# Kernel tuning notes

Measured on AMD Instinct MI355X. Metric: run time of the kernel, lower is better.

The kernel has to match this reference:

```python
import jax, jax.numpy as jnp
import numpy as np

D_MODEL, HEAD_DIM = 1024, 128

def setup_inputs() -> dict:
    key = jax.random.key(0)
    kx, kq, kk, kv = jax.random.split(key, 4)
    x = jax.random.normal(kx, (4, 4096, D_MODEL), dtype=jnp.float32)
    s = 1.0 / np.sqrt(D_MODEL)
    Wq = jax.random.normal(kq, (D_MODEL, HEAD_DIM), dtype=jnp.float32) * s
    Wk = jax.random.normal(kk, (D_MODEL, HEAD_DIM), dtype=jnp.float32) * s
    Wv = jax.random.normal(kv, (D_MODEL, HEAD_DIM), dtype=jnp.float32) * s
    return {"x": x, "Wq": Wq, "Wk": Wk, "Wv": Wv}

def reference(x, Wq, Wk, Wv):
    # x: [b, s, d_model]; Wq/Wk/Wv: [d_model, head_dim]
    q = jnp.einsum('bsd,dh->bsh', x, Wq)
    k = jnp.einsum('bsd,dh->bsh', x, Wk)
    v = jnp.einsum('bsd,dh->bsh', x, Wv)
    seq = x.shape[1]
    scale = 1.0 / jnp.sqrt(jnp.asarray(q.shape[-1], q.dtype))
    scores = jnp.einsum('bqh,bkh->bqk', q, k) * scale  # [b, s, s]
    causal = jnp.tril(jnp.ones((seq, seq), dtype=bool))
    scores = jnp.where(causal, scores, jnp.asarray(-jnp.inf, scores.dtype))
    attn = jax.nn.softmax(scores, axis=-1)
    return jnp.einsum('bqk,bkh->bqh', attn, v)
```

## Files before the change

kernel.cpp:

```cpp
#include <hip/hip_runtime.h>
#include <hip/hip_bf16.h>
#include <math.h>

#define D_MODEL 1024
#define HD 128
#define SEQ 4096

typedef __bf16 bf16x8 __attribute__((ext_vector_type(8)));
typedef float f32x4 __attribute__((ext_vector_type(4)));
typedef unsigned int u32;
typedef u32 u32x4 __attribute__((ext_vector_type(4)));

__device__ __forceinline__ unsigned short f2bf(float f) {
    union { float f; u32 u; } c; c.f = f;
    u32 u = c.u;
    u = (u + 0x7fffu + ((u >> 16) & 1u)) >> 16;
    return (unsigned short)u;
}
__device__ __forceinline__ u32 pk2(float a, float b) {
    __hip_bfloat162 h = __float22bfloat162_rn(make_float2(a, b));
    union { __hip_bfloat162 h; u32 u; } c; c.h = h; return c.u;
}
__device__ __forceinline__ void dma16(void* lds, const void* g) {
    __builtin_amdgcn_global_load_lds(
        (const __attribute__((address_space(1))) u32*)g,
        (__attribute__((address_space(3))) u32*)lds, 16, 0, 0);
}
__device__ __forceinline__ void drain_dma()  { __builtin_amdgcn_s_waitcnt(0x0F70); }
__device__ __forceinline__ void drain_dma4() { __builtin_amdgcn_s_waitcnt(0x0F74); }

__global__ __launch_bounds__(256)
void wt_kernel(const float* __restrict__ Wq, const float* __restrict__ Wk,
               const float* __restrict__ Wv, unsigned short* __restrict__ Wt) {
    __shared__ float wsf[64][129];
    const int t = threadIdx.x;
    const int k0 = blockIdx.x * 64;
    const int mat = blockIdx.y;
    const float* W = (mat == 0) ? Wq : (mat == 1) ? Wk : Wv;
    const float sc = (mat == 0) ? (0.08838834764831845f * 1.4426950408889634f) : 1.0f;
    {
        const int r = t >> 2, c = (t & 3) * 32;
        const float* src = W + (size_t)(k0 + r) * HD + c;
        #pragma unroll
        for (int j = 0; j < 32; j += 4)
            *reinterpret_cast<f32x4*>(&wsf[r][c + j]) = *reinterpret_cast<const f32x4*>(src + j);
    }
    __syncthreads();
    const int n = t >> 1, ks = (t & 1) * 32;
    u32 ow[16];
    #pragma unroll
    for (int j = 0; j < 16; ++j)
        ow[j] = pk2(wsf[ks + 2 * j][n] * sc, wsf[ks + 2 * j + 1][n] * sc);
    unsigned short* dst = Wt + (size_t)(mat * HD + n) * D_MODEL + k0 + ks;
    #pragma unroll
    for (int j = 0; j < 4; ++j)
        *reinterpret_cast<u32x4*>(dst + j * 8) = (u32x4){ow[4*j], ow[4*j+1], ow[4*j+2], ow[4*j+3]};
}

__global__ __launch_bounds__(256)
void proj_kernel(const float* __restrict__ x, const unsigned short* __restrict__ Wt,
                 unsigned short* __restrict__ Qb, unsigned short* __restrict__ Kb,
                 unsigned short* __restrict__ Vt) {
    __shared__ __align__(1024) char ps[49152];
    const int t = threadIdx.x;
    const int w = t >> 6, l = t & 63, li = l & 15, g2 = l >> 4;
    const int id = blockIdx.x;
    const int grp = id / 24, win = id % 24;
    const int nbase = (win >> 3) * 128;
    const int rowbase = (grp * 8 + (win & 7)) * 64;

    f32x4 acc[8];
    #pragma unroll
    for (int nt = 0; nt < 8; ++nt) acc[nt] = (f32x4){0.f, 0.f, 0.f, 0.f};

    const int lrow = l >> 3;
    const int xg = (l & 7) ^ (lrow & 6);
    const int wgr = (l & 7) ^ lrow;
    const int wrow_add = (wgr >> 2) << 6;
    const int wkc = (wgr & 3) * 8;

    auto stage = [&](int k0, int buf) {
        #pragma unroll
        for (int j = 0; j < 2; ++j) {
            int r0 = w * 16 + 8 * j;
            dma16(ps + buf * 8192 + r0 * 128,
                  x + (size_t)(rowbase + r0 + lrow) * D_MODEL + k0 + xg * 4);
            dma16(ps + 24576 + buf * 8192 + r0 * 128,
                  Wt + (size_t)(nbase + r0 + lrow + wrow_add) * D_MODEL + k0 + wkc);
        }
    };

    stage(0, 0);
    stage(32, 1);
    for (int it = 0; it < 32; ++it) {
        const int buf = it % 3;
        if (it < 31) drain_dma4(); else drain_dma();
        __syncthreads();
        if (it + 2 < 32) stage((it + 2) * 32, (it + 2) % 3);
        const char* xb = ps + buf * 8192 + (w * 16 + li) * 128 + (((2 * g2) ^ (li & 6)) * 16);
        f32x4 x0 = *reinterpret_cast<const f32x4*>(xb);
        f32x4 x1 = *reinterpret_cast<const f32x4*>(xb + 16);
        union { u32 d[4]; bf16x8 v; } cva;
        cva.d[0] = pk2(x0[0], x0[1]); cva.d[1] = pk2(x0[2], x0[3]);
        cva.d[2] = pk2(x1[0], x1[1]); cva.d[3] = pk2(x1[2], x1[3]);
        bf16x8 af = cva.v;
        #pragma unroll
        for (int nt = 0; nt < 8; ++nt) {
            bf16x8 bfr = *reinterpret_cast<const bf16x8*>(
                ps + 24576 + buf * 8192 + ((nt & 3) * 16 + li) * 128 +
                ((((nt >> 2) * 4 + g2) ^ (li & 7)) * 16));
            acc[nt] = __builtin_amdgcn_mfma_f32_16x16x32_bf16(af, bfr, acc[nt], 0, 0, 0);
        }
    }

    if (nbase < 256) {
        unsigned short* P = nbase ? Kb : Qb;
        #pragma unroll
        for (int nt = 0; nt < 8; ++nt)
            #pragma unroll
            for (int r = 0; r < 4; ++r) {
                int grow = rowbase + w * 16 + g2 * 4 + r;
                P[(size_t)grow * HD + nt * 16 + li] = f2bf(acc[nt][r]);
            }
    } else {
        int grow0 = rowbase + w * 16 + g2 * 4;
        int b_ = grow0 >> 12, s_ = grow0 & 4095;
        #pragma unroll
        for (int nt = 0; nt < 8; ++nt) {
            ushort4 s4;
            s4.x = f2bf(acc[nt][0]); s4.y = f2bf(acc[nt][1]);
            s4.z = f2bf(acc[nt][2]); s4.w = f2bf(acc[nt][3]);
            *reinterpret_cast<ushort4*>(&Vt[((size_t)b_ * HD + nt * 16 + li) * SEQ + s_]) = s4;
        }
    }
}

__global__ __launch_bounds__(256, 2)
void attn_kernel(const unsigned short* __restrict__ Qb, const unsigned short* __restrict__ Kb,
                 const unsigned short* __restrict__ Vt, float* __restrict__ outO,
                 unsigned short* __restrict__ Obf, float* __restrict__ Lbuf) {
    __shared__ __align__(1024) char smem[36864];
    const int t = threadIdx.x;
    const int w = t >> 6, l = t & 63, li = l & 15, g2 = l >> 4;
    const int b = blockIdx.x & 3;
    const int u = blockIdx.x >> 2;
    const int g = 63 - (u >> 2);
    const int c = u & 3;
    const int R = 2 * g + 2;
    const int ts = (c * R) >> 2, te = ((c + 1) * R) >> 2;
    const int q0 = g * 64;
    const size_t rowb = (size_t)b * SEQ;
    const int qloc = w * 16 + li;

    const unsigned short* KbB = Kb + rowb * HD;
    const unsigned short* VtB = Vt + (size_t)b * HD * SEQ;

    auto stage = [&](int it, char* base) {
        const int j0 = it * 32;
        #pragma unroll
        for (int j = 0; j < 2; ++j) {
            int rK = w * 8 + 4 * j + (l >> 4);
            dma16(base + (w * 8 + 4 * j) * 256,
                  KbB + (size_t)(j0 + rK) * HD + (((l & 15) ^ (rK & 7)) * 8));
            int rV = w * 32 + 16 * j + (l >> 2);
            dma16(base + 8192 + (w * 32 + 16 * j) * 64,
                  VtB + (size_t)rV * SEQ + j0 + (((l & 3) ^ ((l >> 4) & 3)) * 8));
        }
    };

    bf16x8 qf[4];
    #pragma unroll
    for (int ks = 0; ks < 4; ++ks)
        qf[ks] = *reinterpret_cast<const bf16x8*>(
            Qb + (rowb + q0 + qloc) * HD + ks * 32 + g2 * 8);

    f32x4 acco[8];
    #pragma unroll
    for (int dt = 0; dt < 8; ++dt) acco[dt] = (f32x4){0.f, 0.f, 0.f, 0.f};
    float ls = 0.f;

    if (ts < te) stage(ts, smem);
    for (int it = ts; it < te; ++it) {
        char* cbuf = smem + ((it - ts) & 1) * 16384;
        char* nbuf = smem + (((it - ts) & 1) ^ 1) * 16384;
        drain_dma();
        __syncthreads();
        if (it + 1 < te) stage(it + 1, nbuf);

        f32x4 accs[2] = {{0.f,0.f,0.f,0.f}, {0.f,0.f,0.f,0.f}};
        #pragma unroll
        for (int kt = 0; kt < 2; ++kt) {
            const char* kb = cbuf + (kt * 16 + li) * 256;
            #pragma unroll
            for (int ks = 0; ks < 4; ++ks) {
                bf16x8 kf = *reinterpret_cast<const bf16x8*>(kb + (((4 * ks + g2) ^ (li & 7)) * 16));
                accs[kt] = __builtin_amdgcn_mfma_f32_16x16x32_bf16(kf, qf[ks], accs[kt], 0, 0, 0);
            }
        }

        const bool masked = (it >= 2 * g);
        #pragma unroll
        for (int kt = 0; kt < 2; ++kt) {
            float p[4];
            #pragma unroll
            for (int r = 0; r < 4; ++r) {
                float s = accs[kt][r];
                if (masked && ((it - 2 * g) * 32 + kt * 16 + g2 * 4 + r > qloc)) s = -INFINITY;
                p[r] = __builtin_amdgcn_exp2f(s - 16.0f);
                ls += p[r];
            }
            union { u32 d[2]; uint2 v; } pw;
            pw.d[0] = pk2(p[0], p[1]); pw.d[1] = pk2(p[2], p[3]);
            int gq = kt * 2 + (g2 >> 1);
            *reinterpret_cast<uint2*>(
                smem + 32768 + qloc * 64 + ((gq ^ (li & 3)) * 16) + (g2 & 1) * 8) = pw.v;
        }

        bf16x8 pb = *reinterpret_cast<const bf16x8*>(
            smem + 32768 + qloc * 64 + ((g2 ^ (li & 3)) * 16));
        #pragma unroll
        for (int dt = 0; dt < 8; ++dt) {
            bf16x8 va = *reinterpret_cast<const bf16x8*>(
                cbuf + 8192 + (dt * 16 + li) * 64 + ((g2 ^ (li >> 2)) * 16));
            acco[dt] = __builtin_amdgcn_mfma_f32_16x16x32_bf16(va, pb, acco[dt], 0, 0, 0);
        }
    }

    ls += __shfl_xor(ls, 16);
    ls += __shfl_xor(ls, 32);
    if (l < 16)
        Lbuf[(size_t)c * 16384 + rowb + q0 + w * 16 + l] = ls;

    const size_t qrow = rowb + q0 + qloc;
    #pragma unroll
    for (int dt = 0; dt < 8; ++dt) {
        if (c == 3) {
            *reinterpret_cast<f32x4*>(&outO[qrow * HD + dt * 16 + g2 * 4]) = acco[dt];
        } else {
            union { u32 d[2]; uint2 v; } pkd;
            pkd.d[0] = pk2(acco[dt][0], acco[dt][1]);
            pkd.d[1] = pk2(acco[dt][2], acco[dt][3]);
            *reinterpret_cast<uint2*>(
                &Obf[(size_t)c * 2097152 + qrow * HD + dt * 16 + g2 * 4]) = pkd.v;
        }
    }
}

__global__ __launch_bounds__(256)
void merge_kernel(float* __restrict__ outO, const unsigned short* __restrict__ Obf,
                  const float* __restrict__ Lbuf) {
    int tid = blockIdx.x * 256 + threadIdx.x;
    #pragma unroll
    for (int k = 0; k < 4; ++k) {
        int idx = tid + k * 131072;
        int row = idx >> 5, col = (idx & 31) * 4;
        float lsum = Lbuf[row] + Lbuf[16384 + row] + Lbuf[32768 + row] + Lbuf[49152 + row];
        float inv = 1.f / lsum;
        f32x4 o = *reinterpret_cast<const f32x4*>(&outO[(size_t)row * HD + col]);
        #pragma unroll
        for (int cc = 0; cc < 3; ++cc) {
            ushort4 uu = *reinterpret_cast<const ushort4*>(
                &Obf[(size_t)cc * 2097152 + (size_t)row * HD + col]);
            union { u32 u; float f; } a, b2, c2, d2;
            a.u = (u32)uu.x << 16; b2.u = (u32)uu.y << 16;
            c2.u = (u32)uu.z << 16; d2.u = (u32)uu.w << 16;
            o[0] += a.f; o[1] += b2.f; o[2] += c2.f; o[3] += d2.f;
        }
        #pragma unroll
        for (int j = 0; j < 4; ++j) o[j] *= inv;
        *reinterpret_cast<f32x4*>(&outO[(size_t)row * HD + col]) = o;
    }
}

extern "C" void kernel_launch(void* const* d_in, const int* in_sizes, int n_in,
                              void* d_out, int out_size, void* d_ws, size_t ws_size,
                              hipStream_t stream) {
    const float* x  = (const float*)d_in[0];
    const float* Wq = (const float*)d_in[1];
    const float* Wk = (const float*)d_in[2];
    const float* Wv = (const float*)d_in[3];
    float* out = (float*)d_out;

    char* ws = (char*)d_ws;
    unsigned short* Qb  = (unsigned short*)(ws);
    unsigned short* Kb  = (unsigned short*)(ws + ((size_t)4  << 20));
    unsigned short* Vt  = (unsigned short*)(ws + ((size_t)8  << 20));
    unsigned short* Wt  = (unsigned short*)(ws + ((size_t)12 << 20));
    unsigned short* Obf = (unsigned short*)(ws + ((size_t)13 << 20));
    float*          Lb  = (float*)(ws + ((size_t)25 << 20));

    wt_kernel   <<<dim3(16, 3), dim3(256), 0, stream>>>(Wq, Wk, Wv, Wt);
    proj_kernel <<<dim3(768),   dim3(256), 0, stream>>>(x, Wt, Qb, Kb, Vt);
    attn_kernel <<<dim3(1024),  dim3(256), 0, stream>>>(Qb, Kb, Vt, out, Obf, Lb);
    merge_kernel<<<dim3(512),   dim3(256), 0, stream>>>(out, Obf, Lb);
}
```

Before: 171.8 us.

## Fuse split-KV merge into attention kernel via last-block atomic counter

Removes the separate merge kernel launch. Each attention block bumps a per-query-tile atomic counter after a release fence, and the fourth block to finish combines the four partial outputs and row sums for its 64 query rows. The counters are zeroed in the weight-transpose kernel. This saves a launch and lets the merge overlap with the tail of the attention work, at the cost of atomics, fences and an extra tail on some blocks.

Result: slower. 316.6 us (+84.3%).

```diff
diff --git a/kernel.cpp b/kernel.cpp
--- a/kernel.cpp
+++ b/kernel.cpp
@@ -31,9 +31,11 @@
 
 __global__ __launch_bounds__(256)
 void wt_kernel(const float* __restrict__ Wq, const float* __restrict__ Wk,
-               const float* __restrict__ Wv, unsigned short* __restrict__ Wt) {
+               const float* __restrict__ Wv, unsigned short* __restrict__ Wt,
+               int* __restrict__ cnt) {
     __shared__ float wsf[64][129];
     const int t = threadIdx.x;
+    if (blockIdx.x == 0 && blockIdx.y == 0) cnt[t] = 0;
     const int k0 = blockIdx.x * 64;
     const int mat = blockIdx.y;
     const float* W = (mat == 0) ? Wq : (mat == 1) ? Wk : Wv;
@@ -138,7 +140,8 @@
 __global__ __launch_bounds__(256, 2)
 void attn_kernel(const unsigned short* __restrict__ Qb, const unsigned short* __restrict__ Kb,
                  const unsigned short* __restrict__ Vt, float* __restrict__ outO,
-                 unsigned short* __restrict__ Obf, float* __restrict__ Lbuf) {
+                 unsigned short* __restrict__ Obf, float* __restrict__ Lbuf,
+                 int* __restrict__ cnt) {
     __shared__ __align__(1024) char smem[36864];
     const int t = threadIdx.x;
     const int w = t >> 6, l = t & 63, li = l & 15, g2 = l >> 4;
@@ -244,23 +247,30 @@
                 &Obf[(size_t)c * 2097152 + qrow * HD + dt * 16 + g2 * 4]) = pkd.v;
         }
     }
-}
-
-__global__ __launch_bounds__(256)
-void merge_kernel(float* __restrict__ outO, const unsigned short* __restrict__ Obf,
-                  const float* __restrict__ Lbuf) {
-    int tid = blockIdx.x * 256 + threadIdx.x;
-    #pragma unroll
-    for (int k = 0; k < 4; ++k) {
-        int idx = tid + k * 131072;
+
+    __builtin_amdgcn_fence(__ATOMIC_RELEASE, "agent");
+    __syncthreads();
+    __shared__ int lastf;
+    const int gidx = ((u >> 2) << 2) | b;
+    if (t == 0)
+        lastf = (__hip_atomic_fetch_add(&cnt[gidx], 1, __ATOMIC_ACQ_REL,
+                                        __HIP_MEMORY_SCOPE_AGENT) == 3);
+    __syncthreads();
+    if (!lastf) return;
+    __builtin_amdgcn_fence(__ATOMIC_ACQUIRE, "agent");
+
+    #pragma unroll
+    for (int k = 0; k < 8; ++k) {
+        int idx = t + k * 256;
         int row = idx >> 5, col = (idx & 31) * 4;
-        float lsum = Lbuf[row] + Lbuf[16384 + row] + Lbuf[32768 + row] + Lbuf[49152 + row];
+        size_t grow = rowb + q0 + row;
+        float lsum = Lbuf[grow] + Lbuf[16384 + grow] + Lbuf[32768 + grow] + Lbuf[49152 + grow];
         float inv = 1.f / lsum;
-        f32x4 o = *reinterpret_cast<const f32x4*>(&outO[(size_t)row * HD + col]);
+        f32x4 o = *reinterpret_cast<const f32x4*>(&outO[grow * HD + col]);
         #pragma unroll
         for (int cc = 0; cc < 3; ++cc) {
             ushort4 uu = *reinterpret_cast<const ushort4*>(
-                &Obf[(size_t)cc * 2097152 + (size_t)row * HD + col]);
+                &Obf[(size_t)cc * 2097152 + grow * HD + col]);
             union { u32 u; float f; } a, b2, c2, d2;
             a.u = (u32)uu.x << 16; b2.u = (u32)uu.y << 16;
             c2.u = (u32)uu.z << 16; d2.u = (u32)uu.w << 16;
@@ -268,7 +278,7 @@
         }
         #pragma unroll
         for (int j = 0; j < 4; ++j) o[j] *= inv;
-        *reinterpret_cast<f32x4*>(&outO[(size_t)row * HD + col]) = o;
+        *reinterpret_cast<f32x4*>(&outO[grow * HD + col]) = o;
     }
 }
 
@@ -288,9 +298,9 @@
     unsigned short* Wt  = (unsigned short*)(ws + ((size_t)12 << 20));
     unsigned short* Obf = (unsigned short*)(ws + ((size_t)13 << 20));
     float*          Lb  = (float*)(ws + ((size_t)25 << 20));
-
-    wt_kernel   <<<dim3(16, 3), dim3(256), 0, stream>>>(Wq, Wk, Wv, Wt);
+    int*            cnt = (int*)(ws + ((size_t)25 << 20) + (256 << 10));
+
+    wt_kernel   <<<dim3(16, 3), dim3(256), 0, stream>>>(Wq, Wk, Wv, Wt, cnt);
     proj_kernel <<<dim3(768),   dim3(256), 0, stream>>>(x, Wt, Qb, Kb, Vt);
-    attn_kernel <<<dim3(1024),  dim3(256), 0, stream>>>(Qb, Kb, Vt, out, Obf, Lb);
-    merge_kernel<<<dim3(512),   dim3(256), 0, stream>>>(out, Obf, Lb);
-}
+    attn_kernel <<<dim3(1024),  dim3(256), 0, stream>>>(Qb, Kb, Vt, out, Obf, Lb, cnt);
+}
```
